# Kernel tuning notes

Measured on AMD Instinct MI355X. Metric: run time of the kernel, lower is better.

## Reference

```python
import jax, jax.numpy as jnp
import numpy as np

TOP_K = 8


def setup_inputs() -> dict:
    key = jax.random.key(0)
    ks = jax.random.split(key, 6)
    B, S, D, F, E = 2, 1024, 1024, 512, 64
    x = jax.random.normal(ks[0], (B, S, D), dtype=jnp.float32)
    # keras 'random_normal' initializer (stddev=0.05) for centroids
    centroids = jax.random.normal(ks[1], (E, D), dtype=jnp.float32) * 0.05
    expert_biases = jnp.zeros((E,), dtype=jnp.float32)
    # glorot-ish scaling for dense kernels
    Ws_up = jax.random.normal(ks[2], (D, F), dtype=jnp.float32) / np.sqrt(D)
    Ws_down = jax.random.normal(ks[3], (F, D), dtype=jnp.float32) / np.sqrt(F)
    W_up = jax.random.normal(ks[4], (E, D, F), dtype=jnp.float32) / np.sqrt(D)
    W_down = jax.random.normal(ks[5], (E, F, D), dtype=jnp.float32) / np.sqrt(F)
    return {"x": x, "centroids": centroids, "expert_biases": expert_biases,
            "Ws_up": Ws_up, "Ws_down": Ws_down, "W_up": W_up, "W_down": W_down}


def reference(x, centroids, expert_biases, Ws_up, Ws_down, W_up, W_down):
    B, S, D = x.shape
    E = centroids.shape[0]
    T = B * S
    xf = x.reshape(T, D)  # flatten tokens

    # shared expert (num_shared_experts = 1), swish activation, no bias
    shared = jax.nn.silu(xf @ Ws_up) @ Ws_down  # [T, D]

    # affinity routing: top-k on bias-adjusted scores, weights from raw scores
    aff = xf @ centroids.T                        # [T, E]
    biased = aff + expert_biases
    _, idx = jax.lax.top_k(biased, TOP_K)         # [T, K] int32
    sel = jnp.take_along_axis(aff, idx, axis=1)   # gather unbiased scores
    w = jax.nn.sigmoid(sel)
    w = w / (jnp.sum(w, axis=-1, keepdims=True) + 1e-8)  # [T, K]

    # dense combine weights [T, E] (zero where expert not selected)
    cw = jnp.zeros((T, E), dtype=x.dtype).at[jnp.arange(T)[:, None], idx].add(w)

    # routed experts: dense dispatch (equivalent math to masked per-expert FFN)
    h = jax.nn.silu(jnp.einsum('td,edf->etf', xf, W_up))   # [E, T, F]
    y = jnp.einsum('etf,efd->etd', h, W_down)              # [E, T, D]
    routed = jnp.einsum('etd,te->td', y, cw)               # weighted combine

    return (shared + routed).reshape(B, S, D)
```

## Files before the change

kernel.cpp:

```cpp
#include <hip/hip_runtime.h>
#include <math.h>

typedef _Float16 f16;
typedef _Float16 f16x2 __attribute__((ext_vector_type(2)));
typedef _Float16 f16x4 __attribute__((ext_vector_type(4)));
typedef _Float16 f16x8 __attribute__((ext_vector_type(8)));
typedef float f32x4 __attribute__((ext_vector_type(4)));

#define T_TOK 2048
#define DDIM  1024
#define FDIM  512
#define NEXP  64
#define TOPK  8
#define NPAIR (T_TOK * TOPK)
#define NSHT  (T_TOK / 128)
#define MAXTILES 192
#define HPROWS (NPAIR + T_TOK)

static constexpr size_t OFF_XH   = 0;
static constexpr size_t OFF_AFF  = OFF_XH  + (size_t)T_TOK * DDIM * 2;
static constexpr size_t OFF_HPA  = OFF_AFF + (size_t)T_TOK * NEXP * 4;
static constexpr size_t OFF_IDX  = OFF_HPA + (size_t)HPROWS * FDIM * 2;
static constexpr size_t OFF_WB   = OFF_IDX + (size_t)NPAIR * 4;
static constexpr size_t OFF_CNT  = OFF_WB  + (size_t)NPAIR * 4;
static constexpr size_t OFF_OFFS = OFF_CNT + 256;
static constexpr size_t OFF_FILL = OFF_OFFS + 512;
static constexpr size_t OFF_NTS  = OFF_FILL + 256;
static constexpr size_t OFF_TOK  = OFF_NTS + 256;
static constexpr size_t OFF_PW   = OFF_TOK + (size_t)HPROWS * 4;
static constexpr size_t OFF_DESC = OFF_PW  + (size_t)HPROWS * 4;

__device__ __forceinline__ void async_ld16(void* lds, const void* g) {
  __builtin_amdgcn_global_load_lds(
      (const __attribute__((address_space(1))) void*)g,
      (__attribute__((address_space(3))) void*)lds, 16, 0, 0);
}

__global__ void zero_cnt_kernel(int* cnt) {
  if (threadIdx.x < NEXP) cnt[threadIdx.x] = 0;
}

__global__ __launch_bounds__(256)
void aff_kernel(const float* __restrict__ x, const float* __restrict__ cent,
                float* __restrict__ aff, f16* __restrict__ xh) {
  __shared__ __align__(16) float xs[32 * 132];
  __shared__ __align__(16) float cs[64 * 128];
  const int tid = threadIdx.x;
  const int t0 = blockIdx.x * 32;
  const int tg = tid >> 4;
  const int eg = tid & 15;
  float acc0[4] = {0.f, 0.f, 0.f, 0.f};
  float acc1[4] = {0.f, 0.f, 0.f, 0.f};
  for (int kc = 0; kc < DDIM / 128; ++kc) {
    const int kbase = kc * 128;
#pragma unroll
    for (int p = 0; p < 4; ++p) {
      int u = tid + p * 256;
      int row = u >> 5, kk4 = u & 31;
      float4 v = *(const float4*)(x + (size_t)(t0 + row) * DDIM + kbase + kk4 * 4);
      *(float4*)&xs[row * 132 + kk4 * 4] = v;
      f16x4 h = {(f16)v.x, (f16)v.y, (f16)v.z, (f16)v.w};
      *(f16x4*)(xh + (size_t)(t0 + row) * DDIM + kbase + kk4 * 4) = h;
    }
#pragma unroll
    for (int p = 0; p < 8; ++p) {
      int u = tid + p * 256;
      int e = u >> 5, kk4 = u & 31;
      float4 v = *(const float4*)(cent + (size_t)e * DDIM + kbase + kk4 * 4);
      *(float4*)&cs[e * 128 + ((kk4 ^ ((e >> 2) & 7)) << 2)] = v;
    }
    __syncthreads();
#pragma unroll 4
    for (int kk4 = 0; kk4 < 32; ++kk4) {
      float4 xa0 = *(const float4*)&xs[tg * 132 + kk4 * 4];
      float4 xa1 = *(const float4*)&xs[(tg + 16) * 132 + kk4 * 4];
#pragma unroll
      for (int j = 0; j < 4; ++j) {
        int e = eg * 4 + j;
        float4 cb = *(const float4*)&cs[e * 128 + ((kk4 ^ (eg & 7)) << 2)];
        acc0[j] += xa0.x * cb.x + xa0.y * cb.y + xa0.z * cb.z + xa0.w * cb.w;
        acc1[j] += xa1.x * cb.x + xa1.y * cb.y + xa1.z * cb.z + xa1.w * cb.w;
      }
    }
    __syncthreads();
  }
  float4 o0 = {acc0[0], acc0[1], acc0[2], acc0[3]};
  float4 o1 = {acc1[0], acc1[1], acc1[2], acc1[3]};
  *(float4*)(aff + (size_t)(t0 + tg) * NEXP + eg * 4) = o0;
  *(float4*)(aff + (size_t)(t0 + tg + 16) * NEXP + eg * 4) = o1;
}

__global__ __launch_bounds__(256)
void topk_kernel(const float* __restrict__ aff, const float* __restrict__ bias,
                 int* __restrict__ idxbuf, float* __restrict__ wbuf,
                 int* __restrict__ cnt) {
  int tid = threadIdx.x;
  int lane = tid & 63, sub = tid >> 6;
  int token = blockIdx.x * 4 + sub;
  float a = aff[(size_t)token * NEXP + lane];
  float sc = a + bias[lane];
  bool picked = false;
  int selidx = 0;
  for (int p = 0; p < TOPK; ++p) {
    float v = picked ? -3.0e38f : sc;
    int ix = lane;
#pragma unroll
    for (int off = 32; off; off >>= 1) {
      float ov = __shfl_xor(v, off);
      int oi = __shfl_xor(ix, off);
      if (ov > v || (ov == v && oi < ix)) { v = ov; ix = oi; }
    }
    if (lane == ix) picked = true;
    if (lane == p) selidx = ix;
  }
  float rawa = __shfl(a, selidx);
  float s = 1.f / (1.f + expf(-rawa));
  float sum = s;
  sum += __shfl_xor(sum, 1); sum += __shfl_xor(sum, 2); sum += __shfl_xor(sum, 4);
  float wg = s / (sum + 1e-8f);
  if (lane < TOPK) {
    idxbuf[token * TOPK + lane] = selidx;
    wbuf[token * TOPK + lane] = wg;
    atomicAdd(&cnt[selidx], 1);
  }
}

__global__ void scan_desc_kernel(const int* __restrict__ cnt, int* __restrict__ offs,
                                 int* __restrict__ fill, int4* __restrict__ desc,
                                 int* __restrict__ nts) {
  if (threadIdx.x < NEXP) fill[threadIdx.x] = 0;
  if (threadIdx.x == 0) {
    int acc = 0, nt = 0;
    for (int e = 0; e < NEXP; ++e) {
      offs[e] = acc;
      int c = cnt[e];
      for (int r = 0; r < c; r += 128)
        desc[nt++] = make_int4(e, acc + r, min(128, c - r), 0);
      acc += c;
    }
    offs[NEXP] = acc;
    nts[1] = nt;
    for (int i = 0; i < NSHT; ++i)
      desc[nt++] = make_int4(NEXP, NPAIR + i * 128, 128, 0);
    nts[0] = nt;
  }
}

__global__ void scatter_kernel(const int* __restrict__ idxbuf, const float* __restrict__ wbuf,
                               const int* __restrict__ offs, int* __restrict__ fill,
                               int* __restrict__ tokb, float* __restrict__ pwb) {
  int gid = blockIdx.x * 256 + threadIdx.x;
  if (gid < NPAIR) {
    int t = gid >> 3;
    int e = idxbuf[gid];
    int pos = offs[e] + atomicAdd(&fill[e], 1);
    tokb[pos] = t;
    pwb[pos] = wbuf[gid];
  } else {
    tokb[gid] = gid - NPAIR;
    pwb[gid] = 1.0f;
  }
}

template <int MODE, bool GATHER_A>
__global__ __launch_bounds__(256)
void gemm_kernel(const f16* __restrict__ A, const float* __restrict__ Bmat,
                 const float* __restrict__ B2, const int K, const int ldb,
                 const int4* __restrict__ desc, const int* __restrict__ ntiles,
                 const int* __restrict__ tok, const float* __restrict__ pw,
                 void* __restrict__ Out, const int ldo, const long estride) {
  int bx = blockIdx.x, by = blockIdx.y;
  int e = 0, row0, nrows;
  if (desc) {
    if (bx >= *ntiles) return;
    int4 dsc = desc[bx];
    e = dsc.x; row0 = dsc.y; nrows = dsc.z;
  } else {
    row0 = bx * 128; nrows = 128;
  }
  const int n0 = by * 128;
  const float* Bp = (e == NEXP) ? (B2 + n0) : (Bmat + (long)e * estride + n0);

  __shared__ __align__(16) f16 As[128 * 32];
  __shared__ __align__(16) f16 Bs[128 * 40];

  const int tid = threadIdx.x;
  const int rA0 = tid >> 2, rA1 = (tid + 256) >> 2;
  const int kq0 = (tid & 3) * 8;
  const int lr0 = min(rA0, nrows - 1), lr1 = min(rA1, nrows - 1);
  long tg0, tg1;
  if (GATHER_A) { tg0 = tok[row0 + lr0]; tg1 = tok[row0 + lr1]; }
  else          { tg0 = row0 + lr0;      tg1 = row0 + lr1; }
  const f16* a0 = A + tg0 * K + kq0;
  const f16* a1 = A + tg1 * K + kq0;
  const int ukp = tid & 15, un4 = tid >> 4;
  const float* bg = Bp + (size_t)(2 * ukp) * ldb + un4 * 4;
  f16x2* bsw = (f16x2*)Bs;

  f32x4 acc[4][4] = {};
  const int lane = tid & 63, w = tid >> 6;
  const int wro = (w >> 1) * 64, wco = (w & 1) * 64;
  const int fr = lane & 15, kg = (lane >> 4) * 8;

  for (int k0 = 0; k0 < K; k0 += 32) {
    async_ld16(As + tid * 8,        a0 + k0);
    async_ld16(As + tid * 8 + 2048, a1 + k0);
    const float* bgk = bg + (size_t)k0 * ldb;
    float4 v0 = *(const float4*)bgk;
    float4 v1 = *(const float4*)(bgk + ldb);
    float4 v2 = *(const float4*)(bgk + 64);
    float4 v3 = *(const float4*)(bgk + ldb + 64);
#pragma unroll
    for (int i = 0; i < 4; ++i) {
      float a0i = (i == 0) ? v0.x : (i == 1) ? v0.y : (i == 2) ? v0.z : v0.w;
      float b0i = (i == 0) ? v1.x : (i == 1) ? v1.y : (i == 2) ? v1.z : v1.w;
      float a1i = (i == 0) ? v2.x : (i == 1) ? v2.y : (i == 2) ? v2.z : v2.w;
      float b1i = (i == 0) ? v3.x : (i == 1) ? v3.y : (i == 2) ? v3.z : v3.w;
      bsw[(un4 * 4 + i) * 20 + ukp]        = f16x2{(f16)a0i, (f16)b0i};
      bsw[((un4 + 16) * 4 + i) * 20 + ukp] = f16x2{(f16)a1i, (f16)b1i};
    }
    __syncthreads();
    f16x8 af[4], bf[4];
#pragma unroll
    for (int i = 0; i < 4; ++i)
      af[i] = *(const f16x8*)(As + (wro + i * 16 + fr) * 32 + kg);
#pragma unroll
    for (int j = 0; j < 4; ++j)
      bf[j] = *(const f16x8*)(Bs + (wco + j * 16 + fr) * 40 + kg);
#pragma unroll
    for (int i = 0; i < 4; ++i)
#pragma unroll
      for (int j = 0; j < 4; ++j)
        acc[i][j] = __builtin_amdgcn_mfma_f32_16x16x32_f16(af[i], bf[j], acc[i][j], 0, 0, 0);
    __syncthreads();
  }

#pragma unroll
  for (int i = 0; i < 4; ++i) {
    const int mb = wro + i * 16 + (lane >> 4) * 4;
#pragma unroll
    for (int r = 0; r < 4; ++r) {
      const int m = mb + r;
      if (m >= nrows) continue;
      const long gr = row0 + m;
      float wv = 0.f; long orow = 0;
      if (MODE == 2) { wv = pw[gr]; orow = tok[gr]; }
#pragma unroll
      for (int j = 0; j < 4; ++j) {
        const int col = n0 + wco + j * 16 + fr;
        float v = acc[i][j][r];
        if (MODE == 0) {
          float sv = v / (1.f + expf(-v));
          ((f16*)Out)[gr * ldo + col] = (f16)sv;
        } else if (MODE == 1) {
          ((float*)Out)[gr * ldo + col] = v;
        } else {
          atomicAdd((float*)Out + orow * (long)ldo + col, v * wv);
        }
      }
    }
  }
}

extern "C" void kernel_launch(void* const* d_in, const int* in_sizes, int n_in,
                              void* d_out, int out_size, void* d_ws, size_t ws_size,
                              hipStream_t stream) {
  const float* x    = (const float*)d_in[0];
  const float* cent = (const float*)d_in[1];
  const float* bias = (const float*)d_in[2];
  const float* Wsup = (const float*)d_in[3];
  const float* Wsdn = (const float*)d_in[4];
  const float* Wup  = (const float*)d_in[5];
  const float* Wdn  = (const float*)d_in[6];

  char* ws = (char*)d_ws;
  f16*   xh   = (f16*)(ws + OFF_XH);
  float* aff  = (float*)(ws + OFF_AFF);
  f16*   hpa  = (f16*)(ws + OFF_HPA);
  int*   idx  = (int*)(ws + OFF_IDX);
  float* wb   = (float*)(ws + OFF_WB);
  int*   cnt  = (int*)(ws + OFF_CNT);
  int*   offs = (int*)(ws + OFF_OFFS);
  int*   fill = (int*)(ws + OFF_FILL);
  int*   nts  = (int*)(ws + OFF_NTS);
  int*   tokb = (int*)(ws + OFF_TOK);
  float* pwb  = (float*)(ws + OFF_PW);
  int4*  desc = (int4*)(ws + OFF_DESC);
  float* out  = (float*)d_out;

  zero_cnt_kernel<<<1, 64, 0, stream>>>(cnt);
  aff_kernel<<<T_TOK / 32, 256, 0, stream>>>(x, cent, aff, xh);
  topk_kernel<<<T_TOK / 4, 256, 0, stream>>>(aff, bias, idx, wb, cnt);
  scan_desc_kernel<<<1, 64, 0, stream>>>(cnt, offs, fill, desc, nts);
  scatter_kernel<<<HPROWS / 256, 256, 0, stream>>>(idx, wb, offs, fill, tokb, pwb);

  gemm_kernel<0, true><<<dim3(MAXTILES + NSHT, FDIM / 128), 256, 0, stream>>>(
      xh, Wup, Wsup, DDIM, FDIM, desc, &nts[0], tokb, nullptr, hpa, FDIM,
      (long)DDIM * FDIM);
  gemm_kernel<1, false><<<dim3(T_TOK / 128, DDIM / 128), 256, 0, stream>>>(
      hpa + (size_t)NPAIR * FDIM, Wsdn, nullptr, FDIM, DDIM,
      nullptr, nullptr, nullptr, nullptr, out, DDIM, 0);
  gemm_kernel<2, false><<<dim3(MAXTILES, DDIM / 128), 256, 0, stream>>>(
      hpa, Wdn, nullptr, FDIM, DDIM, desc, &nts[1], tokb, pwb, out, DDIM,
      (long)FDIM * DDIM);
}
```

Baseline: 571.0 us.

## Double-buffer GEMM tiles, merge shared down-proj, replace atomics with gather combine

The GEMM main loop now double-buffers the A and B tiles in LDS so the next k-slice loads while the MFMAs run. The A staging layout is also changed. The shared-expert and routed down-projections become one grouped GEMM that writes fp16 per-pair outputs. A new combine kernel then gathers each token's eight weighted rows plus the shared row, replacing float atomicAdd scatter into the output. The affinity GEMM is split along K across four blocks, which accumulate with atomics into a pre-zeroed buffer. This trades atomic contention and serial K loops for an extra fp16 intermediate buffer and more kernel launches.

Result: faster. 520.5 us (-8.9%).

```diff
diff --git a/kernel.cpp b/kernel.cpp
--- a/kernel.cpp
+++ b/kernel.cpp
@@ -20,15 +20,16 @@
 static constexpr size_t OFF_XH   = 0;
 static constexpr size_t OFF_AFF  = OFF_XH  + (size_t)T_TOK * DDIM * 2;
 static constexpr size_t OFF_HPA  = OFF_AFF + (size_t)T_TOK * NEXP * 4;
-static constexpr size_t OFF_IDX  = OFF_HPA + (size_t)HPROWS * FDIM * 2;
+static constexpr size_t OFF_YP   = OFF_HPA + (size_t)HPROWS * FDIM * 2;
+static constexpr size_t OFF_IDX  = OFF_YP  + (size_t)HPROWS * DDIM * 2;
 static constexpr size_t OFF_WB   = OFF_IDX + (size_t)NPAIR * 4;
-static constexpr size_t OFF_CNT  = OFF_WB  + (size_t)NPAIR * 4;
+static constexpr size_t OFF_POS  = OFF_WB  + (size_t)NPAIR * 4;
+static constexpr size_t OFF_CNT  = OFF_POS + (size_t)NPAIR * 4;
 static constexpr size_t OFF_OFFS = OFF_CNT + 256;
 static constexpr size_t OFF_FILL = OFF_OFFS + 512;
 static constexpr size_t OFF_NTS  = OFF_FILL + 256;
 static constexpr size_t OFF_TOK  = OFF_NTS + 256;
-static constexpr size_t OFF_PW   = OFF_TOK + (size_t)HPROWS * 4;
-static constexpr size_t OFF_DESC = OFF_PW  + (size_t)HPROWS * 4;
+static constexpr size_t OFF_DESC = OFF_TOK + (size_t)HPROWS * 4;
 
 __device__ __forceinline__ void async_ld16(void* lds, const void* g) {
   __builtin_amdgcn_global_load_lds(
@@ -36,8 +37,10 @@
       (__attribute__((address_space(3))) void*)lds, 16, 0, 0);
 }
 
-__global__ void zero_cnt_kernel(int* cnt) {
-  if (threadIdx.x < NEXP) cnt[threadIdx.x] = 0;
+__global__ void zero_kernel(float* __restrict__ aff, int* __restrict__ cnt) {
+  int i = blockIdx.x * 256 + threadIdx.x;
+  if (i < T_TOK * NEXP / 4) ((float4*)aff)[i] = float4{0.f, 0.f, 0.f, 0.f};
+  if (blockIdx.x == 0 && threadIdx.x < NEXP) cnt[threadIdx.x] = 0;
 }
 
 __global__ __launch_bounds__(256)
@@ -47,11 +50,12 @@
   __shared__ __align__(16) float cs[64 * 128];
   const int tid = threadIdx.x;
   const int t0 = blockIdx.x * 32;
+  const int kc0 = blockIdx.y * 2;
   const int tg = tid >> 4;
   const int eg = tid & 15;
   float acc0[4] = {0.f, 0.f, 0.f, 0.f};
   float acc1[4] = {0.f, 0.f, 0.f, 0.f};
-  for (int kc = 0; kc < DDIM / 128; ++kc) {
+  for (int kc = kc0; kc < kc0 + 2; ++kc) {
     const int kbase = kc * 128;
 #pragma unroll
     for (int p = 0; p < 4; ++p) {
@@ -84,10 +88,11 @@
     }
     __syncthreads();
   }
-  float4 o0 = {acc0[0], acc0[1], acc0[2], acc0[3]};
-  float4 o1 = {acc1[0], acc1[1], acc1[2], acc1[3]};
-  *(float4*)(aff + (size_t)(t0 + tg) * NEXP + eg * 4) = o0;
-  *(float4*)(aff + (size_t)(t0 + tg + 16) * NEXP + eg * 4) = o1;
+#pragma unroll
+  for (int j = 0; j < 4; ++j) {
+    atomicAdd(aff + (size_t)(t0 + tg) * NEXP + eg * 4 + j, acc0[j]);
+    atomicAdd(aff + (size_t)(t0 + tg + 16) * NEXP + eg * 4 + j, acc1[j]);
+  }
 }
 
 __global__ __launch_bounds__(256)
@@ -128,18 +133,19 @@
 __global__ void scan_desc_kernel(const int* __restrict__ cnt, int* __restrict__ offs,
                                  int* __restrict__ fill, int4* __restrict__ desc,
                                  int* __restrict__ nts) {
-  if (threadIdx.x < NEXP) fill[threadIdx.x] = 0;
+  __shared__ int c[NEXP];
+  if (threadIdx.x < NEXP) { c[threadIdx.x] = cnt[threadIdx.x]; fill[threadIdx.x] = 0; }
+  __syncthreads();
   if (threadIdx.x == 0) {
     int acc = 0, nt = 0;
     for (int e = 0; e < NEXP; ++e) {
       offs[e] = acc;
-      int c = cnt[e];
-      for (int r = 0; r < c; r += 128)
-        desc[nt++] = make_int4(e, acc + r, min(128, c - r), 0);
-      acc += c;
+      int cc = c[e];
+      for (int r = 0; r < cc; r += 128)
+        desc[nt++] = make_int4(e, acc + r, min(128, cc - r), 0);
+      acc += cc;
     }
     offs[NEXP] = acc;
-    nts[1] = nt;
     for (int i = 0; i < NSHT; ++i)
       desc[nt++] = make_int4(NEXP, NPAIR + i * 128, 128, 0);
     nts[0] = nt;
@@ -148,17 +154,31 @@
 
 __global__ void scatter_kernel(const int* __restrict__ idxbuf, const float* __restrict__ wbuf,
                                const int* __restrict__ offs, int* __restrict__ fill,
-                               int* __restrict__ tokb, float* __restrict__ pwb) {
+                               int* __restrict__ tokb, int* __restrict__ posb) {
   int gid = blockIdx.x * 256 + threadIdx.x;
   if (gid < NPAIR) {
     int t = gid >> 3;
     int e = idxbuf[gid];
     int pos = offs[e] + atomicAdd(&fill[e], 1);
     tokb[pos] = t;
-    pwb[pos] = wbuf[gid];
+    posb[gid] = pos;
   } else {
     tokb[gid] = gid - NPAIR;
-    pwb[gid] = 1.0f;
+  }
+}
+
+__device__ __forceinline__ void store_b(f16* Bsbuf, int un4, int ukp,
+                                        const float4& v0, const float4& v1,
+                                        const float4& v2, const float4& v3) {
+  f16x2* bsw = (f16x2*)Bsbuf;
+#pragma unroll
+  for (int i = 0; i < 4; ++i) {
+    float a0i = (i == 0) ? v0.x : (i == 1) ? v0.y : (i == 2) ? v0.z : v0.w;
+    float b0i = (i == 0) ? v1.x : (i == 1) ? v1.y : (i == 2) ? v1.z : v1.w;
+    float a1i = (i == 0) ? v2.x : (i == 1) ? v2.y : (i == 2) ? v2.z : v2.w;
+    float b1i = (i == 0) ? v3.x : (i == 1) ? v3.y : (i == 2) ? v3.z : v3.w;
+    bsw[(un4 * 4 + i) * 20 + ukp]        = f16x2{(f16)a0i, (f16)b0i};
+    bsw[((un4 + 16) * 4 + i) * 20 + ukp] = f16x2{(f16)a1i, (f16)b1i};
   }
 }
 
@@ -167,71 +187,76 @@
 void gemm_kernel(const f16* __restrict__ A, const float* __restrict__ Bmat,
                  const float* __restrict__ B2, const int K, const int ldb,
                  const int4* __restrict__ desc, const int* __restrict__ ntiles,
-                 const int* __restrict__ tok, const float* __restrict__ pw,
-                 void* __restrict__ Out, const int ldo, const long estride) {
-  int bx = blockIdx.x, by = blockIdx.y;
-  int e = 0, row0, nrows;
-  if (desc) {
-    if (bx >= *ntiles) return;
-    int4 dsc = desc[bx];
-    e = dsc.x; row0 = dsc.y; nrows = dsc.z;
-  } else {
-    row0 = bx * 128; nrows = 128;
-  }
+                 const int* __restrict__ tok, void* __restrict__ Out,
+                 const int ldo, const long estride) {
+  const int bx = blockIdx.x, by = blockIdx.y;
+  if (bx >= *ntiles) return;
+  int4 dsc = desc[bx];
+  const int e = dsc.x, row0 = dsc.y, nrows = dsc.z;
   const int n0 = by * 128;
   const float* Bp = (e == NEXP) ? (B2 + n0) : (Bmat + (long)e * estride + n0);
 
-  __shared__ __align__(16) f16 As[128 * 32];
-  __shared__ __align__(16) f16 Bs[128 * 40];
+  __shared__ __align__(16) f16 As[2][128 * 32];
+  __shared__ __align__(16) f16 Bs[2][128 * 40];
 
   const int tid = threadIdx.x;
-  const int rA0 = tid >> 2, rA1 = (tid + 256) >> 2;
-  const int kq0 = (tid & 3) * 8;
-  const int lr0 = min(rA0, nrows - 1), lr1 = min(rA1, nrows - 1);
-  long tg0, tg1;
-  if (GATHER_A) { tg0 = tok[row0 + lr0]; tg1 = tok[row0 + lr1]; }
-  else          { tg0 = row0 + lr0;      tg1 = row0 + lr1; }
-  const f16* a0 = A + tg0 * K + kq0;
-  const f16* a1 = A + tg1 * K + kq0;
+  const int rS = tid & 127;
+  const int kqA = tid >> 7;
+  const int lr = min(rS, nrows - 1);
+  long tg;
+  if (GATHER_A) tg = tok[row0 + lr];
+  else          tg = row0 + lr;
+  const f16* aA = A + tg * K + kqA * 8;
+  const f16* aB = aA + 16;
   const int ukp = tid & 15, un4 = tid >> 4;
   const float* bg = Bp + (size_t)(2 * ukp) * ldb + un4 * 4;
-  f16x2* bsw = (f16x2*)Bs;
 
   f32x4 acc[4][4] = {};
   const int lane = tid & 63, w = tid >> 6;
   const int wro = (w >> 1) * 64, wco = (w & 1) * 64;
   const int fr = lane & 15, kg = (lane >> 4) * 8;
-
-  for (int k0 = 0; k0 < K; k0 += 32) {
-    async_ld16(As + tid * 8,        a0 + k0);
-    async_ld16(As + tid * 8 + 2048, a1 + k0);
-    const float* bgk = bg + (size_t)k0 * ldb;
-    float4 v0 = *(const float4*)bgk;
-    float4 v1 = *(const float4*)(bgk + ldb);
-    float4 v2 = *(const float4*)(bgk + 64);
-    float4 v3 = *(const float4*)(bgk + ldb + 64);
-#pragma unroll
-    for (int i = 0; i < 4; ++i) {
-      float a0i = (i == 0) ? v0.x : (i == 1) ? v0.y : (i == 2) ? v0.z : v0.w;
-      float b0i = (i == 0) ? v1.x : (i == 1) ? v1.y : (i == 2) ? v1.z : v1.w;
-      float a1i = (i == 0) ? v2.x : (i == 1) ? v2.y : (i == 2) ? v2.z : v2.w;
-      float b1i = (i == 0) ? v3.x : (i == 1) ? v3.y : (i == 2) ? v3.z : v3.w;
-      bsw[(un4 * 4 + i) * 20 + ukp]        = f16x2{(f16)a0i, (f16)b0i};
-      bsw[((un4 + 16) * 4 + i) * 20 + ukp] = f16x2{(f16)a1i, (f16)b1i};
-    }
-    __syncthreads();
+  const int aqo = (lane >> 4) * 1024;
+
+  const int NK = K / 32;
+  async_ld16(&As[0][tid * 8], aA);
+  async_ld16(&As[0][(tid + 256) * 8], aB);
+  {
+    float4 v0 = *(const float4*)(bg);
+    float4 v1 = *(const float4*)(bg + ldb);
+    float4 v2 = *(const float4*)(bg + 64);
+    float4 v3 = *(const float4*)(bg + ldb + 64);
+    store_b(Bs[0], un4, ukp, v0, v1, v2, v3);
+  }
+  __syncthreads();
+
+  for (int it = 0; it < NK; ++it) {
+    const int cur = it & 1, nxt = cur ^ 1;
+    const bool more = (it + 1 < NK);
+    float4 w0{}, w1{}, w2{}, w3{};
+    if (more) {
+      const int k0 = (it + 1) * 32;
+      async_ld16(&As[nxt][tid * 8], aA + k0);
+      async_ld16(&As[nxt][(tid + 256) * 8], aB + k0);
+      const float* bgk = bg + (size_t)k0 * ldb;
+      w0 = *(const float4*)(bgk);
+      w1 = *(const float4*)(bgk + ldb);
+      w2 = *(const float4*)(bgk + 64);
+      w3 = *(const float4*)(bgk + ldb + 64);
+    }
     f16x8 af[4], bf[4];
 #pragma unroll
     for (int i = 0; i < 4; ++i)
-      af[i] = *(const f16x8*)(As + (wro + i * 16 + fr) * 32 + kg);
+      af[i] = *(const f16x8*)(&As[cur][aqo + (wro + i * 16 + fr) * 8]);
 #pragma unroll
     for (int j = 0; j < 4; ++j)
-      bf[j] = *(const f16x8*)(Bs + (wco + j * 16 + fr) * 40 + kg);
+      bf[j] = *(const f16x8*)(&Bs[cur][(wco + j * 16 + fr) * 40 + kg]);
 #pragma unroll
     for (int i = 0; i < 4; ++i)
 #pragma unroll
       for (int j = 0; j < 4; ++j)
         acc[i][j] = __builtin_amdgcn_mfma_f32_16x16x32_f16(af[i], bf[j], acc[i][j], 0, 0, 0);
+    if (more)
+      store_b(Bs[nxt], un4, ukp, w0, w1, w2, w3);
     __syncthreads();
   }
 
@@ -243,8 +268,6 @@
       const int m = mb + r;
       if (m >= nrows) continue;
       const long gr = row0 + m;
-      float wv = 0.f; long orow = 0;
-      if (MODE == 2) { wv = pw[gr]; orow = tok[gr]; }
 #pragma unroll
       for (int j = 0; j < 4; ++j) {
         const int col = n0 + wco + j * 16 + fr;
@@ -252,14 +275,35 @@
         if (MODE == 0) {
           float sv = v / (1.f + expf(-v));
           ((f16*)Out)[gr * ldo + col] = (f16)sv;
-        } else if (MODE == 1) {
-          ((float*)Out)[gr * ldo + col] = v;
         } else {
-          atomicAdd((float*)Out + orow * (long)ldo + col, v * wv);
+          ((f16*)Out)[gr * ldo + col] = (f16)v;
         }
       }
     }
   }
+}
+
+__global__ __launch_bounds__(256)
+void combine_kernel(const f16* __restrict__ yp, const int* __restrict__ posb,
+                    const float* __restrict__ wb, float* __restrict__ out) {
+  const int t = blockIdx.x * 2 + (threadIdx.x >> 7);
+  const int d8 = (threadIdx.x & 127) * 8;
+  f16x8 sv = *(const f16x8*)(yp + (size_t)(NPAIR + t) * DDIM + d8);
+  float acc[8];
+#pragma unroll
+  for (int r = 0; r < 8; ++r) acc[r] = (float)sv[r];
+#pragma unroll
+  for (int k = 0; k < TOPK; ++k) {
+    const int pos = posb[t * TOPK + k];
+    const float wk = wb[t * TOPK + k];
+    f16x8 v = *(const f16x8*)(yp + (size_t)pos * DDIM + d8);
+#pragma unroll
+    for (int r = 0; r < 8; ++r) acc[r] += wk * (float)v[r];
+  }
+  float4 o0 = {acc[0], acc[1], acc[2], acc[3]};
+  float4 o1 = {acc[4], acc[5], acc[6], acc[7]};
+  *(float4*)(out + (size_t)t * DDIM + d8) = o0;
+  *(float4*)(out + (size_t)t * DDIM + d8 + 4) = o1;
 }
 
 extern "C" void kernel_launch(void* const* d_in, const int* in_sizes, int n_in,
@@ -277,30 +321,27 @@
   f16*   xh   = (f16*)(ws + OFF_XH);
   float* aff  = (float*)(ws + OFF_AFF);
   f16*   hpa  = (f16*)(ws + OFF_HPA);
+  f16*   yp   = (f16*)(ws + OFF_YP);
   int*   idx  = (int*)(ws + OFF_IDX);
   float* wb   = (float*)(ws + OFF_WB);
+  int*   posb = (int*)(ws + OFF_POS);
   int*   cnt  = (int*)(ws + OFF_CNT);
   int*   offs = (int*)(ws + OFF_OFFS);
   int*   fill = (int*)(ws + OFF_FILL);
   int*   nts  = (int*)(ws + OFF_NTS);
   int*   tokb = (int*)(ws + OFF_TOK);
-  float* pwb  = (float*)(ws + OFF_PW);
   int4*  desc = (int4*)(ws + OFF_DESC);
   float* out  = (float*)d_out;
 
-  zero_cnt_kernel<<<1, 64, 0, stream>>>(cnt);
-  aff_kernel<<<T_TOK / 32, 256, 0, stream>>>(x, cent, aff, xh);
+  zero_kernel<<<T_TOK * NEXP / 4 / 256, 256, 0, stream>>>(aff, cnt);
+  aff_kernel<<<dim3(T_TOK / 32, 4), 256, 0, stream>>>(x, cent, aff, xh);
   topk_kernel<<<T_TOK / 4, 256, 0, stream>>>(aff, bias, idx, wb, cnt);
   scan_desc_kernel<<<1, 64, 0, stream>>>(cnt, offs, fill, desc, nts);
-  scatter_kernel<<<HPROWS / 256, 256, 0, stream>>>(idx, wb, offs, fill, tokb, pwb);
+  scatter_kernel<<<HPROWS / 256, 256, 0, stream>>>(idx, wb, offs, fill, tokb, posb);
 
   gemm_kernel<0, true><<<dim3(MAXTILES + NSHT, FDIM / 128), 256, 0, stream>>>(
-      xh, Wup, Wsup, DDIM, FDIM, desc, &nts[0], tokb, nullptr, hpa, FDIM,
-      (long)DDIM * FDIM);
-  gemm_kernel<1, false><<<dim3(T_TOK / 128, DDIM / 128), 256, 0, stream>>>(
-      hpa + (size_t)NPAIR * FDIM, Wsdn, nullptr, FDIM, DDIM,
-      nullptr, nullptr, nullptr, nullptr, out, DDIM, 0);
-  gemm_kernel<2, false><<<dim3(MAXTILES, DDIM / 128), 256, 0, stream>>>(
-      hpa, Wdn, nullptr, FDIM, DDIM, desc, &nts[1], tokb, pwb, out, DDIM,
-      (long)FDIM * DDIM);
-}
+      xh, Wup, Wsup, DDIM, FDIM, desc, nts, tokb, hpa, FDIM, (long)DDIM * FDIM);
+  gemm_kernel<1, false><<<dim3(MAXTILES + NSHT, DDIM / 128), 256, 0, stream>>>(
+      hpa, Wdn, Wsdn, FDIM, DDIM, desc, nts, tokb, yp, DDIM, (long)FDIM * DDIM);
+  combine_kernel<<<T_TOK / 2, 256, 0, stream>>>(yp, posb, wb, out);
+}
```
